# Kernel tuning notes

Measured on AMD Instinct MI355X. Metric: run time of the kernel, lower is better.

Reference implementation:

```python
import jax, jax.numpy as jnp
import numpy as np

B, N, D, H = 2, 2048, 1024, 16
HD = D // H


def precompute_freqs_cis(dim, end, theta=10000.0):
    freqs = 1.0 / theta ** (jnp.arange(0, dim, 2)[: dim // 2].astype(jnp.float32) / dim)
    t = jnp.arange(end, dtype=jnp.float32)
    freqs = jnp.outer(t, freqs)  # [N, dim//2]
    return jax.lax.complex(jnp.cos(freqs), jnp.sin(freqs))


def apply_rotary(q, k, freqs_cis):
    # q,k: [B,H,N,HD]; freqs_cis: [N, HD//2] broadcasts over B,H
    qr = q.reshape(q.shape[:-1] + (-1, 2))
    kr = k.reshape(k.shape[:-1] + (-1, 2))
    qc = jax.lax.complex(qr[..., 0], qr[..., 1]) * freqs_cis
    kc = jax.lax.complex(kr[..., 0], kr[..., 1]) * freqs_cis
    q_out = jnp.stack([jnp.real(qc), jnp.imag(qc)], axis=-1).reshape(q.shape)
    k_out = jnp.stack([jnp.real(kc), jnp.imag(kc)], axis=-1).reshape(k.shape)
    return q_out, k_out


def setup_inputs() -> dict:
    key = jax.random.key(0)
    ks = jax.random.split(key, 5)
    s = 1.0 / np.sqrt(D)
    return {
        "x": jax.random.normal(ks[0], (B, N, D), dtype=jnp.float32),
        "Wq": jax.random.normal(ks[1], (D, D), dtype=jnp.float32) * s,
        "Wk": jax.random.normal(ks[2], (D, D), dtype=jnp.float32) * s,
        "Wv": jax.random.normal(ks[3], (D, D), dtype=jnp.float32) * s,
        "Wo": jax.random.normal(ks[4], (D, D), dtype=jnp.float32) * s,
    }


def reference(x, Wq, Wk, Wv, Wo):
    b, n, d = x.shape
    h, hd = H, d // H
    q = (x @ Wq).reshape(b, n, h, hd).transpose(0, 2, 1, 3)
    k = (x @ Wk).reshape(b, n, h, hd).transpose(0, 2, 1, 3)
    v = (x @ Wv).reshape(b, n, h, hd).transpose(0, 2, 1, 3)
    freqs_cis = precompute_freqs_cis(hd, n)
    q, k = apply_rotary(q, k, freqs_cis)
    scale = hd ** (-0.5)
    attn = jnp.einsum("bhqd,bhkd->bhqk", q, k) * scale
    attn = jax.nn.softmax(attn, axis=-1)
    out = jnp.einsum("bhqk,bhkd->bhqd", attn, v)
    out = out.transpose(0, 2, 1, 3).reshape(b, n, d)
    return out @ Wo
```

## Files before the change

kernel.cpp:

```cpp
#include <hip/hip_runtime.h>

typedef unsigned short u16;
typedef short  bf16x8 __attribute__((ext_vector_type(8)));
typedef u16    u16x8  __attribute__((ext_vector_type(8)));
typedef float  f32x4  __attribute__((ext_vector_type(4)));
typedef float  f32x2  __attribute__((ext_vector_type(2)));
typedef int    i32x4  __attribute__((ext_vector_type(4)));
typedef unsigned u32x4 __attribute__((ext_vector_type(4)));

__device__ __forceinline__ u16 f2bf(float f) {
  union { float f; unsigned u; } x; x.f = f;
  return (u16)((x.u + 0x7fffu + ((x.u >> 16) & 1u)) >> 16);
}

__device__ __forceinline__ unsigned pk2bf(float a, float b) {
  unsigned r;
  asm("v_cvt_pk_bf16_f32 %0, %1, %2" : "=v"(r) : "v"(a), "v"(b));
  return r;
}

__device__ __forceinline__ float exp2v(float x) {
  float r;
  asm("v_exp_f32 %0, %1" : "=v"(r) : "v"(x));
  return r;
}

__device__ __forceinline__ void gload16(const void* g, void* lds) {
  __builtin_amdgcn_global_load_lds((const __attribute__((address_space(1))) unsigned int*)g,
                                   (__attribute__((address_space(3))) unsigned int*)lds,
                                   16, 0, 0);
}

__device__ __forceinline__ bf16x8 lds8(const u16* base, int row, int colb) {
  int off = (row << 7) + colb;
  off ^= (row & 7) << 4;
  return *(const bf16x8*)((const char*)base + off);
}

__device__ __forceinline__ bf16x8 lds32(const u16* base, int row, int lg) {
  int off = (row << 6) + ((lg ^ ((row >> 1) & 3)) << 4);
  return *(const bf16x8*)((const char*)base + off);
}


__global__ __launch_bounds__(256) void prep_k(const float* __restrict__ x,
                                              const float* __restrict__ Wq,
                                              const float* __restrict__ Wk,
                                              const float* __restrict__ Wv,
                                              const float* __restrict__ Wo,
                                              u16* __restrict__ xb,
                                              u16* __restrict__ WqkvT,
                                              u16* __restrict__ WoT,
                                              f32x2* __restrict__ ctab) {
  __shared__ u16 tile[64][72];
  const int bid = blockIdx.x;
  const int t = threadIdx.x;

  if (bid < 2048) {
    int i = (bid * 256 + t) * 8;
    float4 a = *(const float4*)&x[i];
    float4 b = *(const float4*)&x[i + 4];
    u16x8 o;
    o[0] = f2bf(a.x); o[1] = f2bf(a.y); o[2] = f2bf(a.z); o[3] = f2bf(a.w);
    o[4] = f2bf(b.x); o[5] = f2bf(b.y); o[6] = f2bf(b.z); o[7] = f2bf(b.w);
    *(u16x8*)&xb[i] = o;
  } else if (bid < 3072) {
    int b2 = bid - 2048;
    int z = b2 >> 8, rem = b2 & 255;
    int k0 = (rem >> 4) << 6, nn0 = (rem & 15) << 6;
    const float* W = (z == 0) ? Wq : (z == 1) ? Wk : (z == 2) ? Wv : Wo;
    u16* dst = (z < 3) ? (WqkvT + z * 1024 * 1024) : WoT;
#pragma unroll
    for (int p = 0; p < 4; ++p) {
      int kr = (p << 4) + (t >> 4), c4 = (t & 15) << 2;
      float4 v = *(const float4*)&W[(k0 + kr) * 1024 + nn0 + c4];
      tile[c4 + 0][kr] = f2bf(v.x); tile[c4 + 1][kr] = f2bf(v.y);
      tile[c4 + 2][kr] = f2bf(v.z); tile[c4 + 3][kr] = f2bf(v.w);
    }
    __syncthreads();
#pragma unroll
    for (int p = 0; p < 2; ++p) {
      int nr = (p << 5) + (t >> 3), c8 = (t & 7) << 3;
      i32x4 vv = *(const i32x4*)&tile[nr][c8];
      *(i32x4*)&dst[(nn0 + nr) * 1024 + k0 + c8] = vv;
    }
  } else {
    int idx = (bid - 3072) * 256 + t;
    int i = idx & 31, p = idx >> 5;
    float freq = powf(10000.0f, -(float)(2 * i) * (1.0f / 64.0f));
    float ang = (float)p * freq;
    f32x2 v; v[0] = cosf(ang); v[1] = sinf(ang);
    ctab[idx] = v;
  }
}


__global__ __launch_bounds__(256) void gemm_qkv_k(const u16* __restrict__ A,
                                                  const u16* __restrict__ BT,
                                                  u16* __restrict__ Qb,
                                                  u16* __restrict__ Kb,
                                                  u16* __restrict__ VbT,
                                                  const f32x2* __restrict__ ctab) {
  __shared__ u16 As[3][128 * 32];
  __shared__ u16 Bs[3][128 * 32];
  const int K = 1024;
  const int lin = blockIdx.x;
  const int xcd = lin & 7, idx = lin >> 3;
  const int by = (xcd << 2) + idx / 24;
  const int bx = idx % 24;
  const int m0 = by << 7, n0 = bx << 7;
  const int t = threadIdx.x, w = t >> 6, l = t & 63;
  const int wr = (w >> 1) << 6, wc = (w & 1) << 6;
  const int lr = l & 15, lg = l >> 4;
  const int g_row = l >> 2;
  const int g_col = (((l & 3) ^ ((l >> 3) & 3)) << 3);

  auto stage = [&](int buf, int kt) {
    const int k0_ = kt << 5;
#pragma unroll
    for (int it = 0; it < 2; ++it) {
      int seg = (w << 1) + it;
      int row = (seg << 4) + g_row;
      gload16(&A[(m0 + row) * K + k0_ + g_col], (char*)As[buf] + seg * 1024);
      gload16(&BT[(n0 + row) * K + k0_ + g_col], (char*)Bs[buf] + seg * 1024);
    }
  };

  f32x4 acc[4][4] = {};

  stage(0, 0);
  stage(1, 1);

#pragma unroll
  for (int kt = 0; kt < 32; ++kt) {
    if (kt < 31) asm volatile("s_waitcnt vmcnt(4)" ::: "memory");
    else         asm volatile("s_waitcnt vmcnt(0)" ::: "memory");
    __builtin_amdgcn_s_barrier();
    __builtin_amdgcn_sched_barrier(0);
    if (kt < 30) stage((kt + 2) % 3, kt + 2);
    const u16* Ab = As[kt % 3];
    const u16* Bb = Bs[kt % 3];
    bf16x8 af[4], bfr[4];
#pragma unroll
    for (int m = 0; m < 4; ++m) af[m] = lds32(Ab, wr + (m << 4) + lr, lg);
#pragma unroll
    for (int n = 0; n < 4; ++n) bfr[n] = lds32(Bb, wc + (n << 4) + lr, lg);
#pragma unroll
    for (int m = 0; m < 4; ++m)
#pragma unroll
      for (int n = 0; n < 4; ++n)
        acc[m][n] = __builtin_amdgcn_mfma_f32_16x16x32_bf16(af[m], bfr[n], acc[m][n], 0, 0, 0);
  }

  const int region = n0 >> 10;
  if (region < 2) {
    const float qscale = 0.125f * 1.44269504088896f;
#pragma unroll
    for (int m = 0; m < 4; ++m)
#pragma unroll
      for (int n = 0; n < 4; ++n) {
        const int col = n0 + wc + (n << 4) + lr;
        const int hd = col & 63;
#pragma unroll
        for (int r = 0; r < 4; ++r) {
          const int row = m0 + wr + (m << 4) + (lg << 2) + r;
          float v = acc[m][n][r];
          float p = __shfl_xor(v, 1);
          f32x2 cs = ctab[(row & 2047) * 32 + (hd >> 1)];
          float o = (hd & 1) ? (p * cs[1] + v * cs[0]) : (v * cs[0] - p * cs[1]);
          if (region == 0) { o *= qscale; Qb[row * 1024 + (col & 1023)] = f2bf(o); }
          else             { Kb[row * 1024 + (col & 1023)] = f2bf(o); }
        }
      }
  } else {
#pragma unroll
    for (int m = 0; m < 4; ++m)
#pragma unroll
      for (int n = 0; n < 4; ++n) {
        const int cv = n0 + wc + (n << 4) + lr - 2048;
        const int hh = cv >> 6, dim = cv & 63;
#pragma unroll
        for (int r = 0; r < 4; ++r) {
          const int row = m0 + wr + (m << 4) + (lg << 2) + r;
          const int bb = row >> 11, pos = row & 2047;
          const int k6 = pos & 63;
          const int pp = (k6 & 3) | (((k6 >> 4) & 1) << 2) | (((k6 >> 2) & 3) << 3)
                       | (((k6 >> 5) & 1) << 5);
          const int posp = (pos & ~63) | pp;
          VbT[(((bb << 4) + hh) << 6 | dim) * 2048 + posp] = f2bf(acc[m][n][r]);
        }
      }
  }
}


__global__ __launch_bounds__(256) void gemm_out_k(const u16* __restrict__ A,
                                                  const u16* __restrict__ BT,
                                                  float* __restrict__ C) {
  __shared__ u16 As[3][64 * 32];
  __shared__ u16 Bs[3][128 * 32];
  const int K = 1024;
  const int lin = blockIdx.x;
  const int xcd = lin & 7, idx = lin >> 3;
  const int by = (xcd << 3) + (idx >> 3);
  const int bx = idx & 7;
  const int m0 = by << 6, n0 = bx << 7;
  const int t = threadIdx.x, w = t >> 6, l = t & 63;
  const int wr = (w & 1) << 5, wc = (w >> 1) << 6;
  const int lr = l & 15, lg = l >> 4;
  const int g_row = l >> 2;
  const int g_col = (((l & 3) ^ ((l >> 3) & 3)) << 3);

  auto stage = [&](int buf, int kt) {
    const int k0_ = kt << 5;
    {
      int rowA = (w << 4) + g_row;
      gload16(&A[(m0 + rowA) * K + k0_ + g_col], (char*)As[buf] + w * 1024);
    }
#pragma unroll
    for (int it = 0; it < 2; ++it) {
      int seg = (w << 1) + it;
      int row = (seg << 4) + g_row;
      gload16(&BT[(n0 + row) * K + k0_ + g_col], (char*)Bs[buf] + seg * 1024);
    }
  };

  f32x4 acc[2][4] = {};

  stage(0, 0);
  stage(1, 1);

#pragma unroll
  for (int kt = 0; kt < 32; ++kt) {
    if (kt < 31) asm volatile("s_waitcnt vmcnt(3)" ::: "memory");
    else         asm volatile("s_waitcnt vmcnt(0)" ::: "memory");
    __builtin_amdgcn_s_barrier();
    __builtin_amdgcn_sched_barrier(0);
    if (kt < 30) stage((kt + 2) % 3, kt + 2);
    const u16* Ab = As[kt % 3];
    const u16* Bb = Bs[kt % 3];
    bf16x8 af[2], bfr[4];
#pragma unroll
    for (int m = 0; m < 2; ++m) af[m] = lds32(Ab, wr + (m << 4) + lr, lg);
#pragma unroll
    for (int n = 0; n < 4; ++n) bfr[n] = lds32(Bb, wc + (n << 4) + lr, lg);
#pragma unroll
    for (int m = 0; m < 2; ++m)
#pragma unroll
      for (int n = 0; n < 4; ++n)
        acc[m][n] = __builtin_amdgcn_mfma_f32_16x16x32_bf16(af[m], bfr[n], acc[m][n], 0, 0, 0);
  }

#pragma unroll
  for (int m = 0; m < 2; ++m)
#pragma unroll
    for (int n = 0; n < 4; ++n) {
      const int col = n0 + wc + (n << 4) + lr;
#pragma unroll
      for (int r = 0; r < 4; ++r) {
        const int row = m0 + wr + (m << 4) + (lg << 2) + r;
        C[row * 1024 + col] = acc[m][n][r];
      }
    }
}


__global__ __launch_bounds__(256) void attn_k(const u16* __restrict__ Qb,
                                              const u16* __restrict__ Kb,
                                              const u16* __restrict__ VbT,
                                              u16* __restrict__ Ob) {
  __shared__ u16 Ks[2][2][64 * 64];
  __shared__ u16 Vs[2][2][64 * 64];

  const int lin = blockIdx.x;
  const int xcd = lin & 7, rest = lin >> 3;
  const int bh = (xcd << 2) + (rest & 3);
  const int qt = rest >> 2;
  const int b = bh >> 4;
  const int t = threadIdx.x, w = t >> 6, l = t & 63;
  const int lr = l & 15, lg = l >> 4;
  const int rb = b << 11;
  const int cb = (bh & 15) << 6;
  const int srow = l >> 3;
  const int scol = ((l & 7) ^ srow) << 3;

  auto kv_stage = [&](int buf, int st) {
#pragma unroll
    for (int sub = 0; sub < 2; ++sub) {
      const int tile = (st << 1) + sub;
#pragma unroll
      for (int it = 0; it < 2; ++it) {
        int seg = (w << 1) + it;
        int row = (seg << 3) + srow;
        gload16(&Kb[(size_t)(rb + (tile << 6) + row) * 1024 + cb + scol],
                (char*)Ks[buf][sub] + seg * 1024);
        gload16(&VbT[(size_t)((bh << 6) + row) * 2048 + (tile << 6) + scol],
                (char*)Vs[buf][sub] + seg * 1024);
      }
    }
  };

  bf16x8 qf[2][2];
#pragma unroll
  for (int g = 0; g < 2; ++g)
#pragma unroll
    for (int kk = 0; kk < 2; ++kk)
      qf[g][kk] = *(const bf16x8*)&Qb[(size_t)(rb + (qt << 7) + (w << 5) + (g << 4) + lr) * 1024
                                      + cb + (kk << 5) + (lg << 3)];

  bf16x8 vones;
  {
    u32x4 to; to[0] = 0x3F803F80u; to[1] = 0x3F803F80u; to[2] = 0x3F803F80u; to[3] = 0x3F803F80u;
    vones = *(const bf16x8*)&to;
  }

  kv_stage(0, 0);
  asm volatile("s_waitcnt vmcnt(0)" ::: "memory");
  __builtin_amdgcn_s_barrier();
  __builtin_amdgcn_sched_barrier(0);

  const f32x4 z4 = {0.f, 0.f, 0.f, 0.f};
  f32x4 Osum[2] = {};
  f32x4 Oacc[2][4] = {};

  for (int st = 0; st < 16; ++st) {
    const int buf = st & 1;
    if (st < 15) kv_stage(buf ^ 1, st + 1);

#pragma unroll
    for (int sub = 0; sub < 2; ++sub) {
      const u16* Kc = Ks[buf][sub];
      const u16* Vc = Vs[buf][sub];

      unsigned U[2][4][2];
#pragma unroll
      for (int c = 0; c < 4; ++c) {
        bf16x8 kf0 = lds8(Kc, (c << 4) + lr, (lg << 4));
        bf16x8 kf1 = lds8(Kc, (c << 4) + lr, 64 + (lg << 4));
        f32x4 S[2];
        __builtin_amdgcn_s_setprio(1);
#pragma unroll
        for (int g = 0; g < 2; ++g) {
          S[g] = __builtin_amdgcn_mfma_f32_16x16x32_bf16(kf0, qf[g][0], z4, 0, 0, 0);
          S[g] = __builtin_amdgcn_mfma_f32_16x16x32_bf16(kf1, qf[g][1], S[g], 0, 0, 0);
        }
        __builtin_amdgcn_s_setprio(0);
#pragma unroll
        for (int g = 0; g < 2; ++g) {
          float q0 = exp2v(S[g][0]), q1 = exp2v(S[g][1]);
          float q2 = exp2v(S[g][2]), q3 = exp2v(S[g][3]);
          U[g][c][0] = pk2bf(q0, q1);
          U[g][c][1] = pk2bf(q2, q3);
        }
      }

#pragma unroll
      for (int kk2 = 0; kk2 < 2; ++kk2) {
        bf16x8 vf[4];
#pragma unroll
        for (int df = 0; df < 4; ++df)
          vf[df] = lds8(Vc, (df << 4) + lr, (kk2 << 6) + (lg << 4));
        __builtin_amdgcn_s_setprio(1);
#pragma unroll
        for (int g = 0; g < 2; ++g) {
          u32x4 pt;
          pt[0] = U[g][2 * kk2][0];     pt[1] = U[g][2 * kk2][1];
          pt[2] = U[g][2 * kk2 + 1][0]; pt[3] = U[g][2 * kk2 + 1][1];
          bf16x8 pa = *(const bf16x8*)&pt;
#pragma unroll
          for (int df = 0; df < 4; ++df)
            Oacc[g][df] = __builtin_amdgcn_mfma_f32_16x16x32_bf16(pa, vf[df], Oacc[g][df], 0, 0, 0);
          Osum[g] = __builtin_amdgcn_mfma_f32_16x16x32_bf16(pa, vones, Osum[g], 0, 0, 0);
        }
        __builtin_amdgcn_s_setprio(0);
      }
    }

    asm volatile("s_waitcnt vmcnt(0)" ::: "memory");
    __builtin_amdgcn_s_barrier();
    __builtin_amdgcn_sched_barrier(0);
  }

#pragma unroll
  for (int g = 0; g < 2; ++g) {
    float lq[4];
#pragma unroll
    for (int r = 0; r < 4; ++r) lq[r] = 1.f / Osum[g][r];
#pragma unroll
    for (int df = 0; df < 4; ++df)
#pragma unroll
      for (int r = 0; r < 4; ++r) {
        int row = (qt << 7) + (w << 5) + (g << 4) + (lg << 2) + r;
        int col = (df << 4) + lr;
        Ob[(size_t)(rb + row) * 1024 + cb + col] = f2bf(Oacc[g][df][r] * lq[r]);
      }
  }
}


extern "C" void kernel_launch(void* const* d_in, const int* in_sizes, int n_in,
                              void* d_out, int out_size, void* d_ws, size_t ws_size,
                              hipStream_t stream) {
  const float* x  = (const float*)d_in[0];
  const float* Wq = (const float*)d_in[1];
  const float* Wk = (const float*)d_in[2];
  const float* Wv = (const float*)d_in[3];
  const float* Wo = (const float*)d_in[4];
  float* out = (float*)d_out;

  char* ws = (char*)d_ws;
  u16* xb     = (u16*)(ws);
  u16* WqkvT  = (u16*)(ws + 8388608);
  u16* WoT    = (u16*)(ws + 14680064);
  u16* Qb     = (u16*)(ws + 16777216);
  u16* Kb     = (u16*)(ws + 25165824);
  u16* VbT    = (u16*)(ws + 33554432);
  f32x2* ctab = (f32x2*)(ws + 41943040);
  u16* Ob = xb;

  prep_k<<<3328, 256, 0, stream>>>(x, Wq, Wk, Wv, Wo, xb, WqkvT, WoT, ctab);

  gemm_qkv_k<<<768, 256, 0, stream>>>(xb, WqkvT, Qb, Kb, VbT, ctab);

  attn_k<<<512, 256, 0, stream>>>(Qb, Kb, VbT, Ob);

  gemm_out_k<<<512, 256, 0, stream>>>(Ob, WoT, out);
}
```

Baseline: 110.3 us.

## Switch QKV GEMM to double-buffered BK=64 stages with MFMA priority boost

Changes the QKV projection GEMM from a triple-buffered K=32 pipeline to a double-buffered K=64 pipeline, with a new XOR swizzle for 64-wide rows and lds8 fragment loads. Each stage now does two MFMA sub-steps, so there are half as many barriers. MFMA blocks are also wrapped in s_setprio to favour this wave's matrix issue. The cost is a shallower prefetch distance of one stage, a full vmcnt(0) wait every iteration, and the loop is no longer fully unrolled.

```diff
diff --git a/kernel.cpp b/kernel.cpp
--- a/kernel.cpp
+++ b/kernel.cpp
@@ -101,8 +101,8 @@
                                                   u16* __restrict__ Kb,
                                                   u16* __restrict__ VbT,
                                                   const f32x2* __restrict__ ctab) {
-  __shared__ u16 As[3][128 * 32];
-  __shared__ u16 Bs[3][128 * 32];
+  __shared__ u16 As[2][128 * 64];
+  __shared__ u16 Bs[2][128 * 64];
   const int K = 1024;
   const int lin = blockIdx.x;
   const int xcd = lin & 7, idx = lin >> 3;
@@ -112,44 +112,52 @@
   const int t = threadIdx.x, w = t >> 6, l = t & 63;
   const int wr = (w >> 1) << 6, wc = (w & 1) << 6;
   const int lr = l & 15, lg = l >> 4;
-  const int g_row = l >> 2;
-  const int g_col = (((l & 3) ^ ((l >> 3) & 3)) << 3);
-
-  auto stage = [&](int buf, int kt) {
-    const int k0_ = kt << 5;
-#pragma unroll
-    for (int it = 0; it < 2; ++it) {
-      int seg = (w << 1) + it;
-      int row = (seg << 4) + g_row;
-      gload16(&A[(m0 + row) * K + k0_ + g_col], (char*)As[buf] + seg * 1024);
-      gload16(&BT[(n0 + row) * K + k0_ + g_col], (char*)Bs[buf] + seg * 1024);
+  const int srow = l >> 3;
+  const int scol = ((l & 7) ^ srow) << 3;
+
+  auto stage = [&](int buf, int st) {
+    const int k0_ = st << 6;
+#pragma unroll
+    for (int it = 0; it < 4; ++it) {
+      int seg = (w << 2) + it;
+      int row = (seg << 3) + srow;
+      gload16(&A[(m0 + row) * K + k0_ + scol], (char*)As[buf] + seg * 1024);
+      gload16(&BT[(n0 + row) * K + k0_ + scol], (char*)Bs[buf] + seg * 1024);
     }
   };
 
   f32x4 acc[4][4] = {};
 
   stage(0, 0);
-  stage(1, 1);
-
-#pragma unroll
-  for (int kt = 0; kt < 32; ++kt) {
-    if (kt < 31) asm volatile("s_waitcnt vmcnt(4)" ::: "memory");
-    else         asm volatile("s_waitcnt vmcnt(0)" ::: "memory");
+  asm volatile("s_waitcnt vmcnt(0)" ::: "memory");
+  __builtin_amdgcn_s_barrier();
+  __builtin_amdgcn_sched_barrier(0);
+
+  for (int st = 0; st < 16; ++st) {
+    const int buf = st & 1;
+    if (st < 15) stage(buf ^ 1, st + 1);
+
+    const u16* Ab = As[buf];
+    const u16* Bb = Bs[buf];
+#pragma unroll
+    for (int kk = 0; kk < 2; ++kk) {
+      bf16x8 af[4], bfr[4];
+#pragma unroll
+      for (int m = 0; m < 4; ++m) af[m] = lds8(Ab, wr + (m << 4) + lr, (kk << 6) + (lg << 4));
+#pragma unroll
+      for (int n = 0; n < 4; ++n) bfr[n] = lds8(Bb, wc + (n << 4) + lr, (kk << 6) + (lg << 4));
+      __builtin_amdgcn_s_setprio(1);
+#pragma unroll
+      for (int m = 0; m < 4; ++m)
+#pragma unroll
+        for (int n = 0; n < 4; ++n)
+          acc[m][n] = __builtin_amdgcn_mfma_f32_16x16x32_bf16(af[m], bfr[n], acc[m][n], 0, 0, 0);
+      __builtin_amdgcn_s_setprio(0);
+    }
+
+    asm volatile("s_waitcnt vmcnt(0)" ::: "memory");
     __builtin_amdgcn_s_barrier();
     __builtin_amdgcn_sched_barrier(0);
-    if (kt < 30) stage((kt + 2) % 3, kt + 2);
-    const u16* Ab = As[kt % 3];
-    const u16* Bb = Bs[kt % 3];
-    bf16x8 af[4], bfr[4];
-#pragma unroll
-    for (int m = 0; m < 4; ++m) af[m] = lds32(Ab, wr + (m << 4) + lr, lg);
-#pragma unroll
-    for (int n = 0; n < 4; ++n) bfr[n] = lds32(Bb, wc + (n << 4) + lr, lg);
-#pragma unroll
-    for (int m = 0; m < 4; ++m)
-#pragma unroll
-      for (int n = 0; n < 4; ++n)
-        acc[m][n] = __builtin_amdgcn_mfma_f32_16x16x32_bf16(af[m], bfr[n], acc[m][n], 0, 0, 0);
   }
 
   const int region = n0 >> 10;
```

New measurement: 120.0 us. +8.8%, slower.
